# Kernel optimization log

Hardware: AMD Instinct MI355X
Metric: run time of the kernel (lower is better)

The kernel has to match this reference:

```python
import jax
jax.config.update("jax_enable_x64", True)
import jax.numpy as jnp
import numpy as np

SAMPLE_RATE = 44100
HOP = 512
B, N_MELS, T = 8, 128, 2048
L = T * HOP  # 1,048,576 samples


def _lerp_up(x, out_len):
    # torch F.interpolate(mode='linear', align_corners=True): [B,C,Tin]->[B,C,out_len]
    t_in = x.shape[-1]
    pos = jnp.arange(out_len, dtype=jnp.float64) * ((t_in - 1) / (out_len - 1))
    i0 = jnp.floor(pos).astype(jnp.int32)
    i1 = jnp.minimum(i0 + 1, t_in - 1)
    w = (pos - i0).astype(x.dtype)
    return x[..., i0] * (1 - w) + x[..., i1] * w


def _conv1d(x, w, b, pad):
    y = jax.lax.conv_general_dilated(x, w, (1,), [(pad, pad)],
                                     dimension_numbers=("NCH", "OIH", "NCH"))
    return y + b[None, :, None]


def setup_inputs() -> dict:
    key = jax.random.key(0)
    ks = jax.random.split(key, 9)
    mel_frames = jax.random.normal(ks[0], (B, N_MELS, T), dtype=jnp.float32)
    # realistic f0: 80..380 Hz
    f0_frames = 80.0 + 300.0 * jax.random.uniform(ks[1], (B, T), dtype=jnp.float32)
    noise = jax.random.normal(ks[2], (B, L), dtype=jnp.float32)
    w1 = jax.random.normal(ks[3], (128, N_MELS, 7), dtype=jnp.float32) * 0.05
    b1 = jnp.zeros((128,), jnp.float32)
    w2 = jax.random.normal(ks[4], (128, 128, 3), dtype=jnp.float32) * 0.05
    b2 = jnp.zeros((128,), jnp.float32)
    w3 = jax.random.normal(ks[5], (2, 128, 3), dtype=jnp.float32) * 0.05
    b3 = jnp.zeros((2,), jnp.float32)
    return {"mel_frames": mel_frames, "f0_frames": f0_frames, "noise": noise,
            "w1": w1, "b1": b1, "w2": w2, "b2": b2, "w3": w3, "b3": b3}


def reference(mel_frames, f0_frames, noise, w1, b1, w2, b2, w3, b3):
    # --- comb source ---
    f0 = _lerp_up(f0_frames[:, None, :], L)  # [B,1,L]
    phase = jnp.cumsum(f0.astype(jnp.float64) / SAMPLE_RATE, axis=-1)
    phase = phase - jnp.round(phase)
    phase = phase.astype(f0.dtype)
    combtooth = jnp.sinc(SAMPLE_RATE * phase / (f0 + 1e-8))[:, 0, :]  # [B,L]
    # --- magnitude network ---
    h = jax.nn.leaky_relu(_conv1d(mel_frames, w1, b1, 3), 0.2)
    h = jax.nn.leaky_relu(_conv1d(h, w2, b2, 1), 0.2)
    mags = jnp.clip(_conv1d(h, w3, b3, 1), 0.0, 1.0)  # [B,2,T]
    mags = _lerp_up(mags, L)  # [B,2,L]
    noise_sig = jnp.clip(noise * mags[:, 0, :], -1.0, 1.0)
    comb_sig = jnp.clip(combtooth * mags[:, 1, :], -1.0, 1.0)
    signal = jnp.clip(noise_sig + comb_sig, -1.0, 1.0)
    return (signal[:, None, :], (comb_sig[:, None, :], noise_sig[:, None, :]))
```

## Files before the change

### kernel.cpp

```cpp
#include <hip/hip_runtime.h>
#include <math.h>

#define BATCH 8
#define NMEL 128
#define TT 2048
#define LL 1048576
#define NCHUNK 128
#define CHUNK 8192

static constexpr double RATIO = 2047.0 / 1048575.0;
static constexpr double INV_SR = 1.0 / 44100.0;

__device__ __forceinline__ float f0_at(const float* __restrict__ row, int n) {
    double pos = (double)n * RATIO;
    double fp = floor(pos);
    int i0 = (int)fp;
    int i1 = i0 + 1; if (i1 > TT - 1) i1 = TT - 1;
    float w = (float)(pos - fp);
    return row[i0] * (1.0f - w) + row[i1] * w;
}

__global__ __launch_bounds__(256) void wtrans_kernel(
    const float* __restrict__ w1, const float* __restrict__ w2,
    float* __restrict__ w1t, float* __restrict__ w2t)
{
    int i = blockIdx.x * 256 + threadIdx.x;
    if (i < 896 * 128) {
        int m = i >> 7, co = i & 127;
        w1t[i] = w1[co * 896 + m];
    }
    if (i < 384 * 128) {
        int m = i >> 7, co = i & 127;
        w2t[i] = w2[co * 384 + m];
    }
}

#define XSTR 48
#define HSTR 44
__global__ __launch_bounds__(256, 3) void conv_chunk_kernel(
    const float* __restrict__ mel,
    const float* __restrict__ w1t,
    const float* __restrict__ b1,
    const float* __restrict__ w2t,
    const float* __restrict__ b2,
    const float* __restrict__ w3,
    const float* __restrict__ b3,
    float* __restrict__ mags,
    const float* __restrict__ f0f,
    double* __restrict__ sums)
{
    __shared__ __align__(16) float smem[NMEL * XSTR + NMEL * HSTR + 256];
    int tid = threadIdx.x;

    if (blockIdx.x >= 512) {
        int cb = blockIdx.x - 512;
        int b = cb >> 7;
        int c = cb & (NCHUNK - 1);
        const float* row = f0f + b * TT;
        int start = c * CHUNK + tid * 32;
        double s = 0.0;
        #pragma unroll
        for (int i = 0; i < 32; ++i)
            s += (double)f0_at(row, start + i) * INV_SR;
        double* dred = (double*)smem;
        dred[tid] = s;
        __syncthreads();
        for (int off = 128; off > 0; off >>= 1) {
            if (tid < off) dred[tid] += dred[tid + off];
            __syncthreads();
        }
        if (tid == 0) sums[cb] = dred[0];
        return;
    }

    float* Xs  = smem;
    float* H1  = smem + NMEL * XSTR;
    float* H2  = smem;
    float* red = smem + NMEL * XSTR + NMEL * HSTR;

    int b  = blockIdx.x >> 6;
    int t0 = (blockIdx.x & 63) * 32;
    const float* melb = mel + (size_t)b * NMEL * TT;

    #pragma unroll
    for (int it = 0; it < 6; ++it) {
        int idx = tid + it * 256;
        int ci = idx / 12, q = idx - ci * 12;
        int t = t0 - 8 + q * 4;
        float4 v = make_float4(0.f, 0.f, 0.f, 0.f);
        if (t >= 0 && t + 3 < TT) v = *(const float4*)(melb + ci * TT + t);
        *(float4*)(&Xs[ci * XSTR + q * 4]) = v;
    }
    if (tid < 128) { H1[tid * HSTR + 0] = 0.f; H1[tid * HSTR + 41] = 0.f; }
    __syncthreads();

    int cog = tid >> 3;
    int tg  = tid & 7;
    int xbase = 1 + tg * 5;

    {
        float acc[4][5];
        #pragma unroll
        for (int j = 0; j < 4; ++j) {
            float bj = b1[cog * 4 + j];
            #pragma unroll
            for (int i = 0; i < 5; ++i) acc[j][i] = bj;
        }
        #pragma unroll 2
        for (int ci = 0; ci < NMEL; ++ci) {
            float xv[11];
            #pragma unroll
            for (int i = 0; i < 11; ++i) xv[i] = Xs[ci * XSTR + xbase + i];
            const float* wr = w1t + (size_t)(ci * 7) * 128 + cog * 4;
            #pragma unroll
            for (int k = 0; k < 7; ++k) {
                float4 w4 = *(const float4*)(wr + k * 128);
                float wv[4] = {w4.x, w4.y, w4.z, w4.w};
                #pragma unroll
                for (int j = 0; j < 4; ++j)
                    #pragma unroll
                    for (int i = 0; i < 5; ++i)
                        acc[j][i] = fmaf(wv[j], xv[i + k], acc[j][i]);
            }
        }
        __syncthreads();
        #pragma unroll
        for (int j = 0; j < 4; ++j)
            #pragma unroll
            for (int i = 0; i < 5; ++i) {
                int t = t0 - 4 + tg * 5 + i;
                float v = acc[j][i];
                v = v > 0.0f ? v : 0.2f * v;
                if (t < 0 || t >= TT) v = 0.0f;
                H1[(cog * 4 + j) * HSTR + 1 + tg * 5 + i] = v;
            }
    }
    __syncthreads();

    {
        float acc[4][5];
        #pragma unroll
        for (int j = 0; j < 4; ++j) {
            float bj = b2[cog * 4 + j];
            #pragma unroll
            for (int i = 0; i < 5; ++i) acc[j][i] = bj;
        }
        int hbase = tg * 5;
        #pragma unroll 2
        for (int ci = 0; ci < NMEL; ++ci) {
            float xv[7];
            #pragma unroll
            for (int i = 0; i < 7; ++i) xv[i] = H1[ci * HSTR + hbase + i];
            const float* wr = w2t + (size_t)(ci * 3) * 128 + cog * 4;
            #pragma unroll
            for (int k = 0; k < 3; ++k) {
                float4 w4 = *(const float4*)(wr + k * 128);
                float wv[4] = {w4.x, w4.y, w4.z, w4.w};
                #pragma unroll
                for (int j = 0; j < 4; ++j)
                    #pragma unroll
                    for (int i = 0; i < 5; ++i)
                        acc[j][i] = fmaf(wv[j], xv[i + k], acc[j][i]);
            }
        }
        #pragma unroll
        for (int j = 0; j < 4; ++j)
            #pragma unroll
            for (int i = 0; i < 5; ++i) {
                int t = t0 - 4 + tg * 5 + i;
                float v = acc[j][i];
                v = v > 0.0f ? v : 0.2f * v;
                if (t < 0 || t >= TT) v = 0.0f;
                H2[(cog * 4 + j) * HSTR + tg * 5 + i] = v;
            }
    }
    __syncthreads();

    {
        int o   = tid >> 7;
        int cig = (tid >> 5) & 3;
        int tt  = tid & 31;
        float a = 0.0f;
        for (int cl = 0; cl < 32; ++cl) {
            int ci = cig * 32 + cl;
            #pragma unroll
            for (int k = 0; k < 3; ++k)
                a = fmaf(w3[o * 384 + ci * 3 + k], H2[ci * HSTR + tt + 3 + k], a);
        }
        red[(o * 4 + cig) * 32 + tt] = a;
    }
    __syncthreads();
    if (tid < 64) {
        int o = tid >> 5, tt = tid & 31;
        float s = b3[o] + red[(o * 4 + 0) * 32 + tt] + red[(o * 4 + 1) * 32 + tt]
                        + red[(o * 4 + 2) * 32 + tt] + red[(o * 4 + 3) * 32 + tt];
        s = fminf(fmaxf(s, 0.0f), 1.0f);
        mags[((size_t)b * 2 + o) * TT + t0 + tt] = s;
    }
}

__global__ void scanoff_kernel(const double* __restrict__ sums, double* __restrict__ offs)
{
    int b = threadIdx.x;
    if (b < BATCH) {
        double run = 0.0;
        for (int c = 0; c < NCHUNK; ++c) {
            offs[b * NCHUNK + c] = run;
            run += sums[b * NCHUNK + c];
        }
    }
}

__device__ __forceinline__ int swz4(int g) { return g ^ ((g >> 3) & 7); }

__global__ __launch_bounds__(256, 4) void final_kernel(
    const float* __restrict__ f0f,
    const float* __restrict__ noise,
    const float* __restrict__ mags,
    const double* __restrict__ offs,
    float* __restrict__ out)
{
    int b = blockIdx.x >> 7;
    int c = blockIdx.x & (NCHUNK - 1);
    const float* row = f0f + b * TT;
    int tid = threadIdx.x;
    int lane = tid & 63, wid = tid >> 6;
    __shared__ float4 fracsV[CHUNK / 4];
    __shared__ double wsum[4];

    int chunkBase = c * CHUNK;
    int start = chunkBase + tid * 32;

    float f0v[32];
    double s = 0.0;
    #pragma unroll
    for (int i = 0; i < 32; ++i) {
        f0v[i] = f0_at(row, start + i);
        s += (double)f0v[i] * INV_SR;
    }
    double sinc_ = s;
    #pragma unroll
    for (int off = 1; off < 64; off <<= 1) {
        double v = __shfl_up(sinc_, (unsigned)off, 64);
        if (lane >= off) sinc_ += v;
    }
    if (lane == 63) wsum[wid] = sinc_;
    __syncthreads();
    double run = offs[b * NCHUNK + c] + (sinc_ - s);
    for (int w = 0; w < wid; ++w) run += wsum[w];

    float fb[4];
    #pragma unroll
    for (int i = 0; i < 32; ++i) {
        run += (double)f0v[i] * INV_SR;
        double fr = run - rint(run);
        fb[i & 3] = (float)fr;
        if ((i & 3) == 3)
            fracsV[swz4(tid * 8 + (i >> 2))] = make_float4(fb[0], fb[1], fb[2], fb[3]);
    }
    __syncthreads();

    const size_t BL = (size_t)BATCH * LL;
    const size_t outBase = (size_t)b * LL;
    const float* m0row = mags + (size_t)b * 2 * TT;
    const float* m1row = m0row + TT;

    #pragma unroll 2
    for (int g = 0; g < 8; ++g) {
        int G = g * 256 + tid;
        int n0 = chunkBase + G * 4;
        float4 fr4 = fracsV[swz4(G)];
        const float* frp = (const float*)&fr4;
        float4 nz4 = *(const float4*)(noise + outBase + n0);
        const float* nzp = (const float*)&nz4;

        double pos0 = (double)n0 * RATIO;
        int i0a = (int)floor(pos0);
        int ib = i0a + 1 > TT - 1 ? TT - 1 : i0a + 1;
        int ic = i0a + 2 > TT - 1 ? TT - 1 : i0a + 2;
        float f0a = row[i0a],   f0b = row[ib],   f0c = row[ic];
        float m0a = m0row[i0a], m0b = m0row[ib], m0c = m0row[ic];
        float m1a = m1row[i0a], m1b = m1row[ib], m1c = m1row[ic];

        float so[4], co_[4], no_[4];
        #pragma unroll
        for (int j = 0; j < 4; ++j) {
            double pos = (double)(n0 + j) * RATIO;
            double fp = floor(pos);
            int i0 = (int)fp;
            float w = (float)(pos - fp);
            bool hi = i0 > i0a;
            float xa = hi ? f0b : f0a, xb = hi ? f0c : f0b;
            float f0 = xa * (1.0f - w) + xb * w;
            float ya = hi ? m0b : m0a, yb = hi ? m0c : m0b;
            float m0 = ya * (1.0f - w) + yb * w;
            float za = hi ? m1b : m1a, zb = hi ? m1c : m1b;
            float m1 = za * (1.0f - w) + zb * w;

            float ph = frp[j];
            float x  = 44100.0f * ph * __builtin_amdgcn_rcpf(f0 + 1e-8f);
            float px = 3.14159265358979323f * x;
            float rr = 0.5f * x;
            float rf = rr - rintf(rr);
            float sn;
            asm("v_sin_f32 %0, %1" : "=v"(sn) : "v"(rf));
            float comb = (x == 0.0f) ? 1.0f : sn * __builtin_amdgcn_rcpf(px);

            float ns = fminf(fmaxf(nzp[j] * m0, -1.0f), 1.0f);
            float cs = fminf(fmaxf(comb * m1, -1.0f), 1.0f);
            so[j] = fminf(fmaxf(ns + cs, -1.0f), 1.0f);
            co_[j] = cs; no_[j] = ns;
        }
        *(float4*)(out + outBase + n0)          = make_float4(so[0], so[1], so[2], so[3]);
        *(float4*)(out + BL + outBase + n0)     = make_float4(co_[0], co_[1], co_[2], co_[3]);
        *(float4*)(out + 2 * BL + outBase + n0) = make_float4(no_[0], no_[1], no_[2], no_[3]);
    }
}

extern "C" void kernel_launch(void* const* d_in, const int* in_sizes, int n_in,
                              void* d_out, int out_size, void* d_ws, size_t ws_size,
                              hipStream_t stream) {
    const float* mel   = (const float*)d_in[0];
    const float* f0f   = (const float*)d_in[1];
    const float* noise = (const float*)d_in[2];
    const float* w1    = (const float*)d_in[3];
    const float* b1    = (const float*)d_in[4];
    const float* w2    = (const float*)d_in[5];
    const float* b2    = (const float*)d_in[6];
    const float* w3    = (const float*)d_in[7];
    const float* b3    = (const float*)d_in[8];
    float* out = (float*)d_out;

    float* w1t  = (float*)d_ws;
    float* w2t  = w1t + 896 * 128;
    float* mags = w2t + 384 * 128;
    double* sums = (double*)(mags + BATCH * 2 * TT);
    double* offs = sums + BATCH * NCHUNK;

    wtrans_kernel<<<(896 * 128 + 255) / 256, 256, 0, stream>>>(w1, w2, w1t, w2t);
    conv_chunk_kernel<<<512 + BATCH * NCHUNK, 256, 0, stream>>>(
        mel, w1t, b1, w2t, b2, w3, b3, mags, f0f, sums);
    scanoff_kernel<<<1, 64, 0, stream>>>(sums, offs);
    final_kernel<<<BATCH * NCHUNK, 256, 0, stream>>>(f0f, noise, mags, offs, out);
}
```

Measured before the change: 254.8 us.

## Drop scan kernel, halve chunk size, float interpolation weights, double-buffer conv loads

Removes the serial scanoff kernel by having each final block reduce the preceding chunk sums itself. Halves the chunk size to 4096 so twice as many blocks run. Replaces per-sample double floor interpolation with float incremental weights from a single base position, and uses wave shuffles for the chunk-sum reduction. Software-pipelines the conv1/conv2 channel loops with double-buffered register loads. Float weight accumulation could differ slightly from the double reference at segment boundaries.

```diff
diff --git a/kernel.cpp b/kernel.cpp
--- a/kernel.cpp
+++ b/kernel.cpp
@@ -5,20 +5,12 @@
 #define NMEL 128
 #define TT 2048
 #define LL 1048576
-#define NCHUNK 128
-#define CHUNK 8192
-
-static constexpr double RATIO = 2047.0 / 1048575.0;
+#define NCHUNK 256
+#define CHUNK 4096
+
+static constexpr double RATIO  = 2047.0 / 1048575.0;
+static constexpr float  RATIOF = (float)(2047.0 / 1048575.0);
 static constexpr double INV_SR = 1.0 / 44100.0;
-
-__device__ __forceinline__ float f0_at(const float* __restrict__ row, int n) {
-    double pos = (double)n * RATIO;
-    double fp = floor(pos);
-    int i0 = (int)fp;
-    int i1 = i0 + 1; if (i1 > TT - 1) i1 = TT - 1;
-    float w = (float)(pos - fp);
-    return row[i0] * (1.0f - w) + row[i1] * w;
-}
 
 __global__ __launch_bounds__(256) void wtrans_kernel(
     const float* __restrict__ w1, const float* __restrict__ w2,
@@ -34,6 +26,17 @@
         w2t[i] = w2[co * 384 + m];
     }
 }
+
+#define CONV_FMA(acc, wq, xv, K) \
+    _Pragma("unroll") \
+    for (int k = 0; k < K; ++k) { \
+        float wv0 = wq[k].x, wv1 = wq[k].y, wv2 = wq[k].z, wv3 = wq[k].w; \
+        _Pragma("unroll") \
+        for (int i = 0; i < 5; ++i) { \
+            acc[0][i] = fmaf(wv0, xv[i + k], acc[0][i]); \
+            acc[1][i] = fmaf(wv1, xv[i + k], acc[1][i]); \
+            acc[2][i] = fmaf(wv2, xv[i + k], acc[2][i]); \
+            acc[3][i] = fmaf(wv3, xv[i + k], acc[3][i]); } }
 
 #define XSTR 48
 #define HSTR 44
@@ -49,34 +52,45 @@
     const float* __restrict__ f0f,
     double* __restrict__ sums)
 {
-    __shared__ __align__(16) float smem[NMEL * XSTR + NMEL * HSTR + 256];
+    __shared__ __align__(16) float smem[NMEL * XSTR + NMEL * HSTR];
     int tid = threadIdx.x;
+    int lane = tid & 63, wid = tid >> 6;
 
     if (blockIdx.x >= 512) {
         int cb = blockIdx.x - 512;
-        int b = cb >> 7;
+        int b = cb >> 8;
         int c = cb & (NCHUNK - 1);
         const float* row = f0f + b * TT;
-        int start = c * CHUNK + tid * 32;
+        int start = c * CHUNK + tid * 16;
+        double pos0 = (double)start * RATIO;
+        int i0s = (int)pos0;
+        float wb = (float)(pos0 - (double)i0s);
+        int ib = i0s + 1 > TT - 1 ? TT - 1 : i0s + 1;
+        int ic = i0s + 2 > TT - 1 ? TT - 1 : i0s + 2;
+        float f0a = row[i0s], f0b = row[ib], f0c = row[ic];
         double s = 0.0;
         #pragma unroll
-        for (int i = 0; i < 32; ++i)
-            s += (double)f0_at(row, start + i) * INV_SR;
+        for (int i = 0; i < 16; ++i) {
+            float wi = wb + (float)i * RATIOF;
+            bool hi = wi >= 1.0f;
+            float w = hi ? wi - 1.0f : wi;
+            float xa = hi ? f0b : f0a, xb = hi ? f0c : f0b;
+            float f0 = xa * (1.0f - w) + xb * w;
+            s += (double)f0 * INV_SR;
+        }
+        #pragma unroll
+        for (int off = 32; off > 0; off >>= 1) s += __shfl_down(s, (unsigned)off, 64);
         double* dred = (double*)smem;
-        dred[tid] = s;
+        if (lane == 0) dred[wid] = s;
         __syncthreads();
-        for (int off = 128; off > 0; off >>= 1) {
-            if (tid < off) dred[tid] += dred[tid + off];
-            __syncthreads();
-        }
-        if (tid == 0) sums[cb] = dred[0];
+        if (tid == 0) sums[cb] = dred[0] + dred[1] + dred[2] + dred[3];
         return;
     }
 
     float* Xs  = smem;
     float* H1  = smem + NMEL * XSTR;
     float* H2  = smem;
-    float* red = smem + NMEL * XSTR + NMEL * HSTR;
+    float* red = smem + NMEL * XSTR;
 
     int b  = blockIdx.x >> 6;
     int t0 = (blockIdx.x & 63) * 32;
@@ -106,24 +120,27 @@
             #pragma unroll
             for (int i = 0; i < 5; ++i) acc[j][i] = bj;
         }
-        #pragma unroll 2
-        for (int ci = 0; ci < NMEL; ++ci) {
-            float xv[11];
-            #pragma unroll
-            for (int i = 0; i < 11; ++i) xv[i] = Xs[ci * XSTR + xbase + i];
-            const float* wr = w1t + (size_t)(ci * 7) * 128 + cog * 4;
-            #pragma unroll
-            for (int k = 0; k < 7; ++k) {
-                float4 w4 = *(const float4*)(wr + k * 128);
-                float wv[4] = {w4.x, w4.y, w4.z, w4.w};
-                #pragma unroll
-                for (int j = 0; j < 4; ++j)
-                    #pragma unroll
-                    for (int i = 0; i < 5; ++i)
-                        acc[j][i] = fmaf(wv[j], xv[i + k], acc[j][i]);
-            }
-        }
-        __syncthreads();
+        const float* wb_ = w1t + cog * 4;
+        float xvA[11], xvB[11];
+        float4 wA[7], wB[7];
+        #pragma unroll
+        for (int i = 0; i < 11; ++i) xvA[i] = Xs[xbase + i];
+        #pragma unroll
+        for (int k = 0; k < 7; ++k) wA[k] = *(const float4*)(wb_ + (size_t)k * 128);
+        for (int ci = 0; ci < NMEL; ci += 2) {
+            int c1 = ci + 1;
+            #pragma unroll
+            for (int i = 0; i < 11; ++i) xvB[i] = Xs[c1 * XSTR + xbase + i];
+            #pragma unroll
+            for (int k = 0; k < 7; ++k) wB[k] = *(const float4*)(wb_ + (size_t)(c1 * 7 + k) * 128);
+            CONV_FMA(acc, wA, xvA, 7)
+            int c2 = ci + 2 < NMEL ? ci + 2 : NMEL - 1;
+            #pragma unroll
+            for (int i = 0; i < 11; ++i) xvA[i] = Xs[c2 * XSTR + xbase + i];
+            #pragma unroll
+            for (int k = 0; k < 7; ++k) wA[k] = *(const float4*)(wb_ + (size_t)(c2 * 7 + k) * 128);
+            CONV_FMA(acc, wB, xvB, 7)
+        }
         #pragma unroll
         for (int j = 0; j < 4; ++j)
             #pragma unroll
@@ -146,22 +163,26 @@
             for (int i = 0; i < 5; ++i) acc[j][i] = bj;
         }
         int hbase = tg * 5;
-        #pragma unroll 2
-        for (int ci = 0; ci < NMEL; ++ci) {
-            float xv[7];
-            #pragma unroll
-            for (int i = 0; i < 7; ++i) xv[i] = H1[ci * HSTR + hbase + i];
-            const float* wr = w2t + (size_t)(ci * 3) * 128 + cog * 4;
-            #pragma unroll
-            for (int k = 0; k < 3; ++k) {
-                float4 w4 = *(const float4*)(wr + k * 128);
-                float wv[4] = {w4.x, w4.y, w4.z, w4.w};
-                #pragma unroll
-                for (int j = 0; j < 4; ++j)
-                    #pragma unroll
-                    for (int i = 0; i < 5; ++i)
-                        acc[j][i] = fmaf(wv[j], xv[i + k], acc[j][i]);
-            }
+        const float* wb_ = w2t + cog * 4;
+        float xvA[7], xvB[7];
+        float4 wA[3], wB[3];
+        #pragma unroll
+        for (int i = 0; i < 7; ++i) xvA[i] = H1[hbase + i];
+        #pragma unroll
+        for (int k = 0; k < 3; ++k) wA[k] = *(const float4*)(wb_ + (size_t)k * 128);
+        for (int ci = 0; ci < NMEL; ci += 2) {
+            int c1 = ci + 1;
+            #pragma unroll
+            for (int i = 0; i < 7; ++i) xvB[i] = H1[c1 * HSTR + hbase + i];
+            #pragma unroll
+            for (int k = 0; k < 3; ++k) wB[k] = *(const float4*)(wb_ + (size_t)(c1 * 3 + k) * 128);
+            CONV_FMA(acc, wA, xvA, 3)
+            int c2 = ci + 2 < NMEL ? ci + 2 : NMEL - 1;
+            #pragma unroll
+            for (int i = 0; i < 7; ++i) xvA[i] = H1[c2 * HSTR + hbase + i];
+            #pragma unroll
+            for (int k = 0; k < 3; ++k) wA[k] = *(const float4*)(wb_ + (size_t)(c2 * 3 + k) * 128);
+            CONV_FMA(acc, wB, xvB, 3)
         }
         #pragma unroll
         for (int j = 0; j < 4; ++j)
@@ -199,64 +220,67 @@
     }
 }
 
-__global__ void scanoff_kernel(const double* __restrict__ sums, double* __restrict__ offs)
-{
-    int b = threadIdx.x;
-    if (b < BATCH) {
-        double run = 0.0;
-        for (int c = 0; c < NCHUNK; ++c) {
-            offs[b * NCHUNK + c] = run;
-            run += sums[b * NCHUNK + c];
-        }
-    }
-}
-
 __device__ __forceinline__ int swz4(int g) { return g ^ ((g >> 3) & 7); }
 
 __global__ __launch_bounds__(256, 4) void final_kernel(
     const float* __restrict__ f0f,
     const float* __restrict__ noise,
     const float* __restrict__ mags,
-    const double* __restrict__ offs,
+    const double* __restrict__ sums,
     float* __restrict__ out)
 {
-    int b = blockIdx.x >> 7;
+    int b = blockIdx.x >> 8;
     int c = blockIdx.x & (NCHUNK - 1);
     const float* row = f0f + b * TT;
     int tid = threadIdx.x;
     int lane = tid & 63, wid = tid >> 6;
     __shared__ float4 fracsV[CHUNK / 4];
-    __shared__ double wsum[4];
+    __shared__ double wsumP[4], wsumA[4];
 
     int chunkBase = c * CHUNK;
-    int start = chunkBase + tid * 32;
-
-    float f0v[32];
+    int start = chunkBase + tid * 16;
+
+    double part = (tid < c) ? sums[b * NCHUNK + tid] : 0.0;
+    #pragma unroll
+    for (int off = 32; off > 0; off >>= 1) part += __shfl_down(part, (unsigned)off, 64);
+    if (lane == 0) wsumP[wid] = part;
+
+    double pos0 = (double)start * RATIO;
+    int i0s = (int)pos0;
+    float wb = (float)(pos0 - (double)i0s);
+    int ibk = i0s + 1 > TT - 1 ? TT - 1 : i0s + 1;
+    int ick = i0s + 2 > TT - 1 ? TT - 1 : i0s + 2;
+    float f0a = row[i0s], f0b = row[ibk], f0c = row[ick];
+    float f0v[16];
     double s = 0.0;
     #pragma unroll
-    for (int i = 0; i < 32; ++i) {
-        f0v[i] = f0_at(row, start + i);
+    for (int i = 0; i < 16; ++i) {
+        float wi = wb + (float)i * RATIOF;
+        bool hi = wi >= 1.0f;
+        float w = hi ? wi - 1.0f : wi;
+        float xa = hi ? f0b : f0a, xb = hi ? f0c : f0b;
+        f0v[i] = xa * (1.0f - w) + xb * w;
         s += (double)f0v[i] * INV_SR;
     }
-    double sinc_ = s;
+    double incl = s;
     #pragma unroll
     for (int off = 1; off < 64; off <<= 1) {
-        double v = __shfl_up(sinc_, (unsigned)off, 64);
-        if (lane >= off) sinc_ += v;
-    }
-    if (lane == 63) wsum[wid] = sinc_;
-    __syncthreads();
-    double run = offs[b * NCHUNK + c] + (sinc_ - s);
-    for (int w = 0; w < wid; ++w) run += wsum[w];
+        double v = __shfl_up(incl, (unsigned)off, 64);
+        if (lane >= off) incl += v;
+    }
+    if (lane == 63) wsumA[wid] = incl;
+    __syncthreads();
+    double run = wsumP[0] + wsumP[1] + wsumP[2] + wsumP[3] + (incl - s);
+    for (int w = 0; w < wid; ++w) run += wsumA[w];
 
     float fb[4];
     #pragma unroll
-    for (int i = 0; i < 32; ++i) {
+    for (int i = 0; i < 16; ++i) {
         run += (double)f0v[i] * INV_SR;
         double fr = run - rint(run);
         fb[i & 3] = (float)fr;
         if ((i & 3) == 3)
-            fracsV[swz4(tid * 8 + (i >> 2))] = make_float4(fb[0], fb[1], fb[2], fb[3]);
+            fracsV[swz4(tid * 4 + (i >> 2))] = make_float4(fb[0], fb[1], fb[2], fb[3]);
     }
     __syncthreads();
 
@@ -265,8 +289,8 @@
     const float* m0row = mags + (size_t)b * 2 * TT;
     const float* m1row = m0row + TT;
 
-    #pragma unroll 2
-    for (int g = 0; g < 8; ++g) {
+    #pragma unroll
+    for (int g = 0; g < 4; ++g) {
         int G = g * 256 + tid;
         int n0 = chunkBase + G * 4;
         float4 fr4 = fracsV[swz4(G)];
@@ -274,23 +298,22 @@
         float4 nz4 = *(const float4*)(noise + outBase + n0);
         const float* nzp = (const float*)&nz4;
 
-        double pos0 = (double)n0 * RATIO;
-        int i0a = (int)floor(pos0);
+        double posg = (double)n0 * RATIO;
+        int i0a = (int)posg;
+        float wf = (float)(posg - (double)i0a);
         int ib = i0a + 1 > TT - 1 ? TT - 1 : i0a + 1;
         int ic = i0a + 2 > TT - 1 ? TT - 1 : i0a + 2;
-        float f0a = row[i0a],   f0b = row[ib],   f0c = row[ic];
+        float g0a = row[i0a],   g0b = row[ib],   g0c = row[ic];
         float m0a = m0row[i0a], m0b = m0row[ib], m0c = m0row[ic];
         float m1a = m1row[i0a], m1b = m1row[ib], m1c = m1row[ic];
 
         float so[4], co_[4], no_[4];
         #pragma unroll
         for (int j = 0; j < 4; ++j) {
-            double pos = (double)(n0 + j) * RATIO;
-            double fp = floor(pos);
-            int i0 = (int)fp;
-            float w = (float)(pos - fp);
-            bool hi = i0 > i0a;
-            float xa = hi ? f0b : f0a, xb = hi ? f0c : f0b;
+            float wj = wf + (float)j * RATIOF;
+            bool hi = wj >= 1.0f;
+            float w = hi ? wj - 1.0f : wj;
+            float xa = hi ? g0b : g0a, xb = hi ? g0c : g0b;
             float f0 = xa * (1.0f - w) + xb * w;
             float ya = hi ? m0b : m0a, yb = hi ? m0c : m0b;
             float m0 = ya * (1.0f - w) + yb * w;
@@ -335,11 +358,9 @@
     float* w2t  = w1t + 896 * 128;
     float* mags = w2t + 384 * 128;
     double* sums = (double*)(mags + BATCH * 2 * TT);
-    double* offs = sums + BATCH * NCHUNK;
 
     wtrans_kernel<<<(896 * 128 + 255) / 256, 256, 0, stream>>>(w1, w2, w1t, w2t);
     conv_chunk_kernel<<<512 + BATCH * NCHUNK, 256, 0, stream>>>(
         mel, w1t, b1, w2t, b2, w3, b3, mags, f0f, sums);
-    scanoff_kernel<<<1, 64, 0, stream>>>(sums, offs);
-    final_kernel<<<BATCH * NCHUNK, 256, 0, stream>>>(f0f, noise, mags, offs, out);
+    final_kernel<<<BATCH * NCHUNK, 256, 0, stream>>>(f0f, noise, mags, sums, out);
 }
```

Measured after the change: 261.6 us. 2.7% more time.
